# Performance work log

Hardware: AMD Instinct MI355X
Metric: run time of the kernel (lower is better)

The kernel has to match this reference:

```python
import jax, jax.numpy as jnp
import numpy as np

B, T, D = 2, 2048, 2048
NH, HD = 16, 128
Q_LAT, KV_LAT = 1024, 512
EPS = 1e-6
THETA = 10000.0


def setup_inputs() -> dict:
    key = jax.random.key(0)
    ks = jax.random.split(key, 8)
    x = jax.random.normal(ks[0], (B, T, D), dtype=jnp.float32)
    # causal additive mask, broadcast over batch/heads
    neg = jnp.finfo(jnp.float32).min
    causal = jnp.where(jnp.tril(jnp.ones((T, T), dtype=bool)), 0.0, neg)
    attn_mask = causal[None, None, :, :].astype(jnp.float32)
    s = lambda fan_in: 1.0 / np.sqrt(fan_in)
    q_a_w = jax.random.normal(ks[1], (Q_LAT, D), dtype=jnp.float32) * s(D)
    q_b_w = jax.random.normal(ks[2], (NH * HD, Q_LAT), dtype=jnp.float32) * s(Q_LAT)
    kv_a_w = jax.random.normal(ks[3], (KV_LAT, D), dtype=jnp.float32) * s(D)
    k_b_w = jax.random.normal(ks[4], (NH * HD, KV_LAT), dtype=jnp.float32) * s(KV_LAT)
    v_b_w = jax.random.normal(ks[5], (NH * HD, KV_LAT), dtype=jnp.float32) * s(KV_LAT)
    o_w = jax.random.normal(ks[6], (D, NH * HD), dtype=jnp.float32) * s(NH * HD)
    q_norm_w = jnp.ones((HD,), dtype=jnp.float32)
    k_norm_w = jnp.ones((HD,), dtype=jnp.float32)
    return dict(x=x, attn_mask=attn_mask, q_a_w=q_a_w, q_b_w=q_b_w, kv_a_w=kv_a_w,
                k_b_w=k_b_w, v_b_w=v_b_w, o_w=o_w, q_norm_w=q_norm_w, k_norm_w=k_norm_w)


def _rms_norm(x, w):
    var = jnp.mean(jnp.square(x), axis=-1, keepdims=True)
    return x * jax.lax.rsqrt(var + EPS) * w


def _rope_cache(t, hd, dtype):
    inv_freq = 1.0 / (THETA ** (jnp.arange(0, hd, 2, dtype=jnp.float32) / hd))
    freqs = jnp.arange(t, dtype=jnp.float32)[:, None] * inv_freq[None, :]  # [t, hd/2]
    emb = jnp.concatenate([freqs, freqs], axis=-1)  # [t, hd]
    return jnp.cos(emb).astype(dtype), jnp.sin(emb).astype(dtype)


def _rotate_half(x):
    h = x.shape[-1] // 2
    return jnp.concatenate([-x[..., h:], x[..., :h]], axis=-1)


def reference(x, attn_mask, q_a_w, q_b_w, kv_a_w, k_b_w, v_b_w, o_w, q_norm_w, k_norm_w):
    b, t, d = x.shape
    # low-rank projections (torch Linear: y = x @ W.T)
    q = (x @ q_a_w.T) @ q_b_w.T          # [b, t, nh*hd]
    kv = x @ kv_a_w.T                     # [b, t, kv_lat]
    k = kv @ k_b_w.T
    v = kv @ v_b_w.T
    q = q.reshape(b, t, NH, HD).transpose(0, 2, 1, 3)  # [b, nh, t, hd]
    k = k.reshape(b, t, NH, HD).transpose(0, 2, 1, 3)
    v = v.reshape(b, t, NH, HD).transpose(0, 2, 1, 3)
    # QK-norm over head dim
    q = _rms_norm(q, q_norm_w)
    k = _rms_norm(k, k_norm_w)
    # RoPE
    cos, sin = _rope_cache(t, HD, x.dtype)  # [t, hd]
    cos = cos[None, None, :, :]
    sin = sin[None, None, :, :]
    q = q * cos + _rotate_half(q) * sin
    k = k * cos + _rotate_half(k) * sin
    # attention
    sd = 1.0 / np.sqrt(HD)
    attn = jnp.einsum('bhqd,bhkd->bhqk', q, k) * sd + attn_mask
    attn = jax.nn.softmax(attn, axis=-1)
    out = jnp.einsum('bhqk,bhkd->bhqd', attn, v)
    out = out.transpose(0, 2, 1, 3).reshape(b, t, NH * HD)
    return out @ o_w.T
```

## Files before the change

kernel.cpp:

```cpp
#include <hip/hip_runtime.h>
#include <hip/hip_fp16.h>

typedef _Float16 f16;
typedef _Float16 f16x4 __attribute__((ext_vector_type(4)));
typedef _Float16 f16x8 __attribute__((ext_vector_type(8)));
typedef float f32x4 __attribute__((ext_vector_type(4)));

#define BT 4096
#define DMODEL 2048

__device__ __forceinline__ void gld16(const f16* g, f16* l) {
    __builtin_amdgcn_global_load_lds((const __attribute__((address_space(1))) void*)g,
                                     (__attribute__((address_space(3))) void*)l, 16, 0, 0);
}

struct Cvt7 {
    const float* s[7];
    f16* d[7];
    int off4[8];
};
__global__ __launch_bounds__(256) void k_cvt7(Cvt7 c) {
    int i = blockIdx.x * 256 + threadIdx.x;
    if (i >= c.off4[7]) return;
    int seg = 0;
#pragma unroll
    for (int k = 1; k < 7; ++k) seg += (i >= c.off4[k]);
    int j = i - c.off4[seg];
    float4 v = ((const float4*)c.s[seg])[j];
    f16x4 h;
    h[0] = (f16)v.x; h[1] = (f16)v.y; h[2] = (f16)v.z; h[3] = (f16)v.w;
    ((f16x4*)c.d[seg])[j] = h;
}

template <typename CT>
__global__ __launch_bounds__(256, 3) void k_gemm_bt(const f16* __restrict__ A,
                                                    const f16* __restrict__ Bm,
                                                    CT* __restrict__ C,
                                                    int M, int N, int K) {
    __shared__ __align__(16) char smem[16384];
    f16* Als = (f16*)smem;
    f16* Bls = (f16*)(smem + 8192);
    const int tid = threadIdx.x;
    const int w = tid >> 6, l = tid & 63;
    const int quad = l >> 4, ln = l & 15;
    const int m0 = blockIdx.y * 128, n0 = blockIdx.x * 128;
    const int wm = (w >> 1) * 64, wn = (w & 1) * 64;
    const int srow = l >> 2, scol = (l & 3) * 8;

    f32x4 acc[4][4];
#pragma unroll
    for (int i = 0; i < 4; ++i)
#pragma unroll
        for (int j = 0; j < 4; ++j)
#pragma unroll
            for (int r = 0; r < 4; ++r) acc[i][j][r] = 0.f;

    for (int k0 = 0; k0 < K; k0 += 32) {
#pragma unroll
        for (int c = 0; c < 2; ++c) {
            const int ch = w + 4 * c;
            gld16(A + (size_t)(m0 + ch * 16 + srow) * K + (k0 + scol), &Als[ch * 512]);
            gld16(Bm + (size_t)(n0 + ch * 16 + srow) * K + (k0 + scol), &Bls[ch * 512]);
        }
        __syncthreads();
        f16x8 af[4], bf[4];
#pragma unroll
        for (int i = 0; i < 4; ++i) af[i] = *(const f16x8*)&Als[(wm + 16 * i + ln) * 32 + quad * 8];
#pragma unroll
        for (int j = 0; j < 4; ++j) bf[j] = *(const f16x8*)&Bls[(wn + 16 * j + ln) * 32 + quad * 8];
#pragma unroll
        for (int i = 0; i < 4; ++i)
#pragma unroll
            for (int j = 0; j < 4; ++j)
                acc[i][j] = __builtin_amdgcn_mfma_f32_16x16x32_f16(af[i], bf[j], acc[i][j], 0, 0, 0);
        __syncthreads();
    }
    const int p_w = (w >> 1) ? 16 : 0;
#pragma unroll
    for (int i = 0; i < 4; ++i) {
        if constexpr (sizeof(CT) == 2) {
            f16* Cs = (f16*)smem;
#pragma unroll
            for (int j = 0; j < 4; ++j)
#pragma unroll
                for (int r = 0; r < 4; ++r)
                    Cs[(p_w + quad * 4 + r) * 136 + wn + 16 * j + ln] = (f16)acc[i][j][r];
            __syncthreads();
#pragma unroll
            for (int k2 = 0; k2 < 2; ++k2) {
                int idx = k2 * 256 + tid;
                int pr = idx >> 4, c = idx & 15;
                int rg = m0 + 16 * i + (pr & 15) + ((pr & 16) ? 64 : 0);
                *(f16x8*)&C[(size_t)rg * N + n0 + c * 8] = *(const f16x8*)&Cs[pr * 136 + c * 8];
            }
        } else {
            float* Cs = (float*)smem;
#pragma unroll
            for (int j = 0; j < 4; ++j)
#pragma unroll
                for (int r = 0; r < 4; ++r)
                    Cs[(p_w + quad * 4 + r) * 128 + wn + 16 * j + ln] = acc[i][j][r];
            __syncthreads();
#pragma unroll
            for (int k2 = 0; k2 < 4; ++k2) {
                int idx = k2 * 256 + tid;
                int pr = idx >> 5, c = idx & 31;
                int rg = m0 + 16 * i + (pr & 15) + ((pr & 16) ? 64 : 0);
                *(float4*)&C[(size_t)rg * N + n0 + c * 4] = *(const float4*)&Cs[pr * 128 + c * 4];
            }
        }
        __syncthreads();
    }
}

__global__ __launch_bounds__(256, 3) void k_gemm_dual(const f16* __restrict__ A,
                                                      const f16* __restrict__ B0,
                                                      const f16* __restrict__ B1,
                                                      f16* __restrict__ C0, f16* __restrict__ C1,
                                                      int K, int nsplit, int ld0, int ld1) {
    __shared__ __align__(16) char smem[16384];
    f16* Als = (f16*)smem;
    f16* Bls = (f16*)(smem + 8192);
    const int tid = threadIdx.x;
    const int w = tid >> 6, l = tid & 63;
    const int quad = l >> 4, ln = l & 15;
    const int m0 = blockIdx.y * 128, n0 = blockIdx.x * 128;
    const int wm = (w >> 1) * 64, wn = (w & 1) * 64;
    const int srow = l >> 2, scol = (l & 3) * 8;
    const f16* Bm = (n0 < nsplit) ? B0 + (size_t)n0 * K : B1 + (size_t)(n0 - nsplit) * K;

    f32x4 acc[4][4];
#pragma unroll
    for (int i = 0; i < 4; ++i)
#pragma unroll
        for (int j = 0; j < 4; ++j)
#pragma unroll
            for (int r = 0; r < 4; ++r) acc[i][j][r] = 0.f;

    for (int k0 = 0; k0 < K; k0 += 32) {
#pragma unroll
        for (int c = 0; c < 2; ++c) {
            const int ch = w + 4 * c;
            gld16(A + (size_t)(m0 + ch * 16 + srow) * K + (k0 + scol), &Als[ch * 512]);
            gld16(Bm + (size_t)(ch * 16 + srow) * K + (k0 + scol), &Bls[ch * 512]);
        }
        __syncthreads();
        f16x8 af[4], bf[4];
#pragma unroll
        for (int i = 0; i < 4; ++i) af[i] = *(const f16x8*)&Als[(wm + 16 * i + ln) * 32 + quad * 8];
#pragma unroll
        for (int j = 0; j < 4; ++j) bf[j] = *(const f16x8*)&Bls[(wn + 16 * j + ln) * 32 + quad * 8];
#pragma unroll
        for (int i = 0; i < 4; ++i)
#pragma unroll
            for (int j = 0; j < 4; ++j)
                acc[i][j] = __builtin_amdgcn_mfma_f32_16x16x32_f16(af[i], bf[j], acc[i][j], 0, 0, 0);
        __syncthreads();
    }
    f16* Cd; int ldc, cb;
    if (n0 < nsplit) { Cd = C0; ldc = ld0; cb = n0; }
    else             { Cd = C1; ldc = ld1; cb = n0 - nsplit; }
    const int p_w = (w >> 1) ? 16 : 0;
    f16* Cs = (f16*)smem;
#pragma unroll
    for (int i = 0; i < 4; ++i) {
#pragma unroll
        for (int j = 0; j < 4; ++j)
#pragma unroll
            for (int r = 0; r < 4; ++r)
                Cs[(p_w + quad * 4 + r) * 136 + wn + 16 * j + ln] = (f16)acc[i][j][r];
        __syncthreads();
#pragma unroll
        for (int k2 = 0; k2 < 2; ++k2) {
            int idx = k2 * 256 + tid;
            int pr = idx >> 4, c = idx & 15;
            int rg = m0 + 16 * i + (pr & 15) + ((pr & 16) ? 64 : 0);
            *(f16x8*)&Cd[(size_t)rg * ldc + cb + c * 8] = *(const f16x8*)&Cs[pr * 136 + c * 8];
        }
        __syncthreads();
    }
}

__global__ __launch_bounds__(256, 3) void k_gemm_kv(const f16* __restrict__ A,
                                                    const f16* __restrict__ B0,
                                                    const f16* __restrict__ B1,
                                                    f16* __restrict__ Ck, f16* __restrict__ Vt,
                                                    int K) {
    __shared__ __align__(16) char smem[16384];
    f16* Als = (f16*)smem;
    f16* Bls = (f16*)(smem + 8192);
    const int tid = threadIdx.x;
    const int w = tid >> 6, l = tid & 63;
    const int quad = l >> 4, ln = l & 15;
    const int m0 = blockIdx.y * 128, n0 = blockIdx.x * 128;
    const int wm = (w >> 1) * 64, wn = (w & 1) * 64;
    const int srow = l >> 2, scol = (l & 3) * 8;
    const f16* Bm = (n0 < 2048) ? B0 + (size_t)n0 * K : B1 + (size_t)(n0 - 2048) * K;

    f32x4 acc[4][4];
#pragma unroll
    for (int i = 0; i < 4; ++i)
#pragma unroll
        for (int j = 0; j < 4; ++j)
#pragma unroll
            for (int r = 0; r < 4; ++r) acc[i][j][r] = 0.f;

    for (int k0 = 0; k0 < K; k0 += 32) {
#pragma unroll
        for (int c = 0; c < 2; ++c) {
            const int ch = w + 4 * c;
            gld16(A + (size_t)(m0 + ch * 16 + srow) * K + (k0 + scol), &Als[ch * 512]);
            gld16(Bm + (size_t)(ch * 16 + srow) * K + (k0 + scol), &Bls[ch * 512]);
        }
        __syncthreads();
        f16x8 af[4], bf[4];
#pragma unroll
        for (int i = 0; i < 4; ++i) af[i] = *(const f16x8*)&Als[(wm + 16 * i + ln) * 32 + quad * 8];
#pragma unroll
        for (int j = 0; j < 4; ++j) bf[j] = *(const f16x8*)&Bls[(wn + 16 * j + ln) * 32 + quad * 8];
#pragma unroll
        for (int i = 0; i < 4; ++i)
#pragma unroll
            for (int j = 0; j < 4; ++j)
                acc[i][j] = __builtin_amdgcn_mfma_f32_16x16x32_f16(af[i], bf[j], acc[i][j], 0, 0, 0);
        __syncthreads();
    }
    const int p_w = (w >> 1) ? 16 : 0;
    f16* Cs = (f16*)smem;
    const int bb = m0 >> 11;
    const int tb = m0 & 2047;
#pragma unroll
    for (int i = 0; i < 4; ++i) {
#pragma unroll
        for (int j = 0; j < 4; ++j)
#pragma unroll
            for (int r = 0; r < 4; ++r)
                Cs[(p_w + quad * 4 + r) * 136 + wn + 16 * j + ln] = (f16)acc[i][j][r];
        __syncthreads();
        if (n0 < 2048) {
#pragma unroll
            for (int k2 = 0; k2 < 2; ++k2) {
                int idx = k2 * 256 + tid;
                int pr = idx >> 4, c = idx & 15;
                int rg = m0 + 16 * i + (pr & 15) + ((pr & 16) ? 64 : 0);
                *(f16x8*)&Ck[(size_t)rg * 2048 + n0 + c * 8] = *(const f16x8*)&Cs[pr * 136 + c * 8];
            }
        } else {
#pragma unroll
            for (int it = 0; it < 2; ++it) {
                int idx = it * 256 + tid;
                int d = idx & 127, tc = (idx >> 7) & 1, g = idx >> 8;
                f16x8 v;
#pragma unroll
                for (int k = 0; k < 8; ++k) v[k] = Cs[(g * 16 + tc * 8 + k) * 136 + d];
                int t = tb + 16 * i + g * 64 + tc * 8;
                *(f16x8*)&Vt[((size_t)(bb * 2048 + (n0 - 2048) + d)) * 2048 + t] = v;
            }
        }
        __syncthreads();
    }
}

__global__ __launch_bounds__(512, 2) void k_gemm8f(const f16* __restrict__ A,
                                                   const f16* __restrict__ B0,
                                                   float* __restrict__ C0,
                                                   int K, int ld0) {
    __shared__ __align__(16) f16 lds[49152];
    const int tid = threadIdx.x;
    const int w = tid >> 6, l = tid & 63;
    const int wm = w >> 2, wn = w & 3;
    const int quad = l >> 4, ln = l & 15;
    const int m0 = blockIdx.y * 128, n0 = blockIdx.x * 256;

    const f16* Bp = B0 + (size_t)n0 * K;

    const f16* ag  = A + (size_t)(m0 + w * 16 + (l >> 2)) * K + (l & 3) * 8;
    const f16* bg0 = Bp + (size_t)(w * 16 + (l >> 2)) * K + (l & 3) * 8;
    const f16* bg1 = bg0 + (size_t)128 * K;
    f16* al = &lds[w * 512];
    f16* bl = &lds[4096 + w * 512];

#define STAGE8(buf_, kc_, t_)                          \
    {                                                  \
        const int off_ = ((buf_) * 2 + (kc_)) * 12288; \
        const int g_ = (t_) * 64 + (kc_) * 32;         \
        gld16(ag + g_, al + off_);                     \
        gld16(bg0 + g_, bl + off_);                    \
        gld16(bg1 + g_, bl + off_ + 4096);             \
    }

    f32x4 acc[4][4];
#pragma unroll
    for (int i = 0; i < 4; ++i)
#pragma unroll
        for (int j = 0; j < 4; ++j)
#pragma unroll
            for (int r = 0; r < 4; ++r) acc[i][j][r] = 0.f;

    const int nt = K >> 6;
    STAGE8(0, 0, 0);
    STAGE8(0, 1, 0);
    STAGE8(1, 0, 1);
    asm volatile("s_waitcnt vmcnt(3)" ::: "memory");
    __builtin_amdgcn_s_barrier();
    asm volatile("s_waitcnt lgkmcnt(0)" ::: "memory");

    for (int t = 0; t < nt; ++t) {
        const int buf = t & 1;
#pragma unroll
        for (int kc = 0; kc < 2; ++kc) {
            const f16* Ah = &lds[(buf * 2 + kc) * 12288];
            const f16* Bh = Ah + 4096;
            f16x8 a[4], b[4];
#pragma unroll
            for (int i = 0; i < 4; ++i)
                a[i] = *(const f16x8*)&Ah[(wm * 64 + i * 16 + ln) * 32 + quad * 8];
#pragma unroll
            for (int j = 0; j < 4; ++j)
                b[j] = *(const f16x8*)&Bh[(wn * 64 + j * 16 + ln) * 32 + quad * 8];
            if (kc == 0) {
                if (t + 1 < nt) STAGE8(buf ^ 1, 1, t + 1);
            } else {
                if (t + 2 < nt) STAGE8(buf, 0, t + 2);
            }
            __builtin_amdgcn_s_barrier();
            asm volatile("s_waitcnt lgkmcnt(0)" ::: "memory");
            __builtin_amdgcn_s_setprio(1);
#pragma unroll
            for (int i = 0; i < 4; ++i)
#pragma unroll
                for (int j = 0; j < 4; ++j)
                    acc[i][j] = __builtin_amdgcn_mfma_f32_16x16x32_f16(a[i], b[j], acc[i][j], 0, 0, 0);
            __builtin_amdgcn_s_setprio(0);
            if (kc == 1 && t + 1 < nt) {
                if (t + 2 < nt) asm volatile("s_waitcnt vmcnt(3)" ::: "memory");
                else            asm volatile("s_waitcnt vmcnt(0)" ::: "memory");
            }
            __builtin_amdgcn_s_barrier();
        }
    }
#undef STAGE8

    const int p = (wm ? 16 : 0) + quad * 4;
    float* Cs = (float*)lds;
#pragma unroll
    for (int i = 0; i < 4; ++i) {
        __syncthreads();
#pragma unroll
        for (int j = 0; j < 4; ++j)
#pragma unroll
            for (int r = 0; r < 4; ++r)
                Cs[(p + r) * 260 + wn * 64 + j * 16 + ln] = acc[i][j][r];
        __syncthreads();
#pragma unroll
        for (int rr = 0; rr < 4; ++rr) {
            int idx = rr * 512 + tid;
            int row = idx >> 6, c4 = idx & 63;
            int rg = m0 + i * 16 + (row & 15) + ((row & 16) ? 64 : 0);
            *(float4*)&C0[(size_t)rg * ld0 + n0 + c4 * 4] = *(const float4*)&Cs[row * 260 + c4 * 4];
        }
    }
}

__global__ __launch_bounds__(256) void k_norm_rope(f16* __restrict__ q, f16* __restrict__ k,
                                                   const float* __restrict__ qw,
                                                   const float* __restrict__ kw) {
    const int gw = blockIdx.x * 4 + (threadIdx.x >> 6);
    const int l = threadIdx.x & 63;
    const int which = gw >> 16;
    const int rh = gw & 65535;
    const int row = rh >> 4, h = rh & 15;
    f16* p = which ? k : q;
    const float* wp = which ? kw : qw;
    const float scale = which ? 1.0f : 0.08838834764831843f;
    const size_t base = (size_t)row * DMODEL + h * 128;
    float xa = (float)p[base + l];
    float xb = (float)p[base + 64 + l];
    float ss = xa * xa + xb * xb;
#pragma unroll
    for (int off = 32; off > 0; off >>= 1) ss += __shfl_xor(ss, off);
    const float rms = rsqrtf(ss * (1.0f / 128.0f) + 1e-6f);
    const float na = xa * rms * wp[l];
    const float nb = xb * rms * wp[64 + l];
    const int t = row & 2047;
    const float freq = __expf((float)l * -0.1439115683121279f);
    const float ang = (float)t * freq;
    const float c = cosf(ang), s = sinf(ang);
    p[base + l]      = (f16)((na * c - nb * s) * scale);
    p[base + 64 + l] = (f16)((nb * c + na * s) * scale);
}

__global__ __launch_bounds__(256, 3) void k_flash(const f16* __restrict__ Q, const f16* __restrict__ K,
                                                  const f16* __restrict__ Vt, f16* __restrict__ O) {
    __shared__ f16 Kl[64 * 136];
    __shared__ f16 Vl[128 * 72];
    const int h = blockIdx.x, b = blockIdx.y, mt = 31 - blockIdx.z;
    const int tid = threadIdx.x, w = tid >> 6, l64 = tid & 63;
    const int quad = l64 >> 4, ln = l64 & 15;

    f16x8 qf[4];
    {
        const int tq = mt * 64 + w * 16 + ln;
        const f16* qp = Q + (size_t)(b * 2048 + tq) * DMODEL + h * 128 + quad * 8;
#pragma unroll
        for (int kc = 0; kc < 4; ++kc) qf[kc] = *(const f16x8*)(qp + kc * 32);
    }
    f32x4 oacc[8];
#pragma unroll
    for (int ot = 0; ot < 8; ++ot)
#pragma unroll
        for (int r = 0; r < 4; ++r) oacc[ot][r] = 0.f;
    float m_r = -INFINITY, l_r = 0.f;

    const f16* kbase = K + (size_t)(b * 2048) * DMODEL + h * 128;
    const f16* vbase = Vt + (size_t)(b * 2048 + h * 128) * 2048;

    f16x8 kr[4], vr[4];
#pragma unroll
    for (int c = 0; c < 4; ++c) {
        int idx = c * 256 + tid;
        kr[c] = *(const f16x8*)(kbase + (size_t)(idx >> 4) * DMODEL + (idx & 15) * 8);
        vr[c] = *(const f16x8*)(vbase + (size_t)(idx >> 3) * 2048 + (idx & 7) * 8);
    }

    for (int j = 0; j <= mt; ++j) {
        __syncthreads();
#pragma unroll
        for (int c = 0; c < 4; ++c) {
            int idx = c * 256 + tid;
            *(f16x8*)&Kl[(idx >> 4) * 136 + (idx & 15) * 8] = kr[c];
            *(f16x8*)&Vl[(idx >> 3) * 72 + (idx & 7) * 8] = vr[c];
        }
        __syncthreads();
        if (j < mt) {
#pragma unroll
            for (int c = 0; c < 4; ++c) {
                int idx = c * 256 + tid;
                kr[c] = *(const f16x8*)(kbase + (size_t)((j + 1) * 64 + (idx >> 4)) * DMODEL + (idx & 15) * 8);
                vr[c] = *(const f16x8*)(vbase + (size_t)(idx >> 3) * 2048 + (j + 1) * 64 + (idx & 7) * 8);
            }
        }
        f32x4 sacc[4];
#pragma unroll
        for (int nt = 0; nt < 4; ++nt)
#pragma unroll
            for (int r = 0; r < 4; ++r) sacc[nt][r] = 0.f;
#pragma unroll
        for (int nt = 0; nt < 4; ++nt)
#pragma unroll
            for (int kc = 0; kc < 4; ++kc) {
                f16x8 kf = *(const f16x8*)&Kl[(nt * 16 + ln) * 136 + kc * 32 + quad * 8];
                sacc[nt] = __builtin_amdgcn_mfma_f32_16x16x32_f16(kf, qf[kc], sacc[nt], 0, 0, 0);
            }
        if (j == mt) {
#pragma unroll
            for (int nt = 0; nt < 4; ++nt)
#pragma unroll
                for (int r = 0; r < 4; ++r)
                    if (nt * 16 + quad * 4 + r > w * 16 + ln) sacc[nt][r] = -INFINITY;
        }
        float mx = -INFINITY;
#pragma unroll
        for (int nt = 0; nt < 4; ++nt)
#pragma unroll
            for (int r = 0; r < 4; ++r) mx = fmaxf(mx, sacc[nt][r]);
        mx = fmaxf(mx, __shfl_xor(mx, 16));
        mx = fmaxf(mx, __shfl_xor(mx, 32));
        const bool grow = (mx > m_r + 8.f);
        const float mn = grow ? fmaxf(m_r, mx) : m_r;
        const float alpha = grow ? __expf(m_r - mn) : 1.f;
        m_r = mn;
        f16x4 pa[4];
        float s0 = 0.f;
#pragma unroll
        for (int nt = 0; nt < 4; ++nt)
#pragma unroll
            for (int r = 0; r < 4; ++r) {
                float pv = __expf(sacc[nt][r] - mn);
                s0 += pv;
                pa[nt][r] = (f16)pv;
            }
        s0 += __shfl_xor(s0, 16);
        s0 += __shfl_xor(s0, 32);
        l_r = l_r * alpha + s0;
        if (__ballot(grow)) {
            float ar[4];
#pragma unroll
            for (int r = 0; r < 4; ++r) ar[r] = __shfl(alpha, (l64 & 48) | (quad * 4 + r));
#pragma unroll
            for (int ot = 0; ot < 8; ++ot)
#pragma unroll
                for (int r = 0; r < 4; ++r) oacc[ot][r] *= ar[r];
        }
#pragma unroll
        for (int nt = 0; nt < 4; ++nt)
#pragma unroll
            for (int ot = 0; ot < 8; ++ot) {
                f16x4 vf = *(const f16x4*)&Vl[(ot * 16 + ln) * 72 + nt * 16 + quad * 4];
                oacc[ot] = __builtin_amdgcn_mfma_f32_16x16x16f16(pa[nt], vf, oacc[ot], 0, 0, 0);
            }
    }
    const float inv = 1.0f / l_r;
    float ivr[4];
#pragma unroll
    for (int r = 0; r < 4; ++r) ivr[r] = __shfl(inv, (l64 & 48) | (quad * 4 + r));
    __syncthreads();
#pragma unroll
    for (int ot = 0; ot < 8; ++ot)
#pragma unroll
        for (int r = 0; r < 4; ++r)
            Kl[(w * 16 + quad * 4 + r) * 136 + ot * 16 + ln] = (f16)(oacc[ot][r] * ivr[r]);
    __syncthreads();
#pragma unroll
    for (int c = 0; c < 4; ++c) {
        int idx = c * 256 + tid;
        int row = idx >> 4, col8 = (idx & 15) * 8;
        *(f16x8*)&O[(size_t)(b * 2048 + mt * 64 + row) * DMODEL + h * 128 + col8] =
            *(const f16x8*)&Kl[row * 136 + col8];
    }
}

extern "C" void kernel_launch(void* const* d_in, const int* in_sizes, int n_in,
                              void* d_out, int out_size, void* d_ws, size_t ws_size,
                              hipStream_t stream) {
    const float* x    = (const float*)d_in[0];
    const float* qaw  = (const float*)d_in[2];
    const float* qbw  = (const float*)d_in[3];
    const float* kvaw = (const float*)d_in[4];
    const float* kbw  = (const float*)d_in[5];
    const float* vbw  = (const float*)d_in[6];
    const float* ow   = (const float*)d_in[7];
    const float* qnw  = (const float*)d_in[8];
    const float* knw  = (const float*)d_in[9];
    float* out = (float*)d_out;

    char* p = (char*)d_ws;
    auto alloc = [&](size_t elems) { f16* r = (f16*)p; p += elems * sizeof(f16); return r; };
    f16* xb   = alloc((size_t)BT * 2048);
    f16* wo   = alloc((size_t)2048 * 2048);
    f16* wqa  = alloc((size_t)1024 * 2048);
    f16* wqb  = alloc((size_t)2048 * 1024);
    f16* wkva = alloc((size_t)512 * 2048);
    f16* wkb  = alloc((size_t)2048 * 512);
    f16* wvb  = alloc((size_t)2048 * 512);
    f16* qlat = alloc((size_t)BT * 1024);
    f16* kvb  = alloc((size_t)BT * 512);
    f16* qpre = alloc((size_t)BT * 2048);
    f16* kpre = alloc((size_t)BT * 2048);
    f16* vt   = xb;
    f16* attn = wqa;

    Cvt7 c;
    c.s[0] = x;    c.d[0] = xb;
    c.s[1] = qaw;  c.d[1] = wqa;
    c.s[2] = qbw;  c.d[2] = wqb;
    c.s[3] = kvaw; c.d[3] = wkva;
    c.s[4] = kbw;  c.d[4] = wkb;
    c.s[5] = vbw;  c.d[5] = wvb;
    c.s[6] = ow;   c.d[6] = wo;
    int sz4[7] = {BT * 2048 / 4, 1024 * 2048 / 4, 2048 * 1024 / 4, 512 * 2048 / 4,
                  2048 * 512 / 4, 2048 * 512 / 4, 2048 * 2048 / 4};
    c.off4[0] = 0;
    for (int i = 0; i < 7; ++i) c.off4[i + 1] = c.off4[i] + sz4[i];
    k_cvt7<<<(c.off4[7] + 255) / 256, 256, 0, stream>>>(c);

    dim3 blk(256);
    k_gemm_dual<<<dim3(1536 / 128, BT / 128), blk, 0, stream>>>(xb, wqa, wkva, qlat, kvb, 2048, 1024, 1024, 512);
    k_gemm_bt<f16><<<dim3(2048 / 128, BT / 128), blk, 0, stream>>>(qlat, wqb, qpre, BT, 2048, 1024);
    k_gemm_kv<<<dim3(4096 / 128, BT / 128), blk, 0, stream>>>(kvb, wkb, wvb, kpre, vt, 512);
    k_norm_rope<<<32768, 256, 0, stream>>>(qpre, kpre, qnw, knw);
    k_flash<<<dim3(16, 2, 32), 256, 0, stream>>>(qpre, kpre, vt, attn);
    k_gemm8f<<<dim3(2048 / 256, BT / 128), 512, 0, stream>>>(attn, wo, out, 2048, 2048);
}
```

Before: 394.2 us.

## Route all projection GEMMs through pipelined 128x256 kernel with templated epilogues

Replaces the simple 128x128 single-buffered GEMM kernels for the Q/KV latent, Q up-projection and K/V up-projection with the templated, software-pipelined 512-thread 128x256 kernel previously used only for the output projection. Mode-specific epilogues handle the split outputs, fp16 stores via an LDS staging tile, and a direct transposed V store from registers. This aims to raise MFMA utilisation and cut per-K-step barrier stalls in the earlier GEMMs. The cost is fewer blocks for the small-N GEMM (6x32 grid) and uncoalesced 8-byte transposed V writes.

```diff
diff --git a/kernel.cpp b/kernel.cpp
--- a/kernel.cpp
+++ b/kernel.cpp
@@ -32,239 +32,13 @@
     ((f16x4*)c.d[seg])[j] = h;
 }
 
-template <typename CT>
-__global__ __launch_bounds__(256, 3) void k_gemm_bt(const f16* __restrict__ A,
-                                                    const f16* __restrict__ Bm,
-                                                    CT* __restrict__ C,
-                                                    int M, int N, int K) {
-    __shared__ __align__(16) char smem[16384];
-    f16* Als = (f16*)smem;
-    f16* Bls = (f16*)(smem + 8192);
-    const int tid = threadIdx.x;
-    const int w = tid >> 6, l = tid & 63;
-    const int quad = l >> 4, ln = l & 15;
-    const int m0 = blockIdx.y * 128, n0 = blockIdx.x * 128;
-    const int wm = (w >> 1) * 64, wn = (w & 1) * 64;
-    const int srow = l >> 2, scol = (l & 3) * 8;
-
-    f32x4 acc[4][4];
-#pragma unroll
-    for (int i = 0; i < 4; ++i)
-#pragma unroll
-        for (int j = 0; j < 4; ++j)
-#pragma unroll
-            for (int r = 0; r < 4; ++r) acc[i][j][r] = 0.f;
-
-    for (int k0 = 0; k0 < K; k0 += 32) {
-#pragma unroll
-        for (int c = 0; c < 2; ++c) {
-            const int ch = w + 4 * c;
-            gld16(A + (size_t)(m0 + ch * 16 + srow) * K + (k0 + scol), &Als[ch * 512]);
-            gld16(Bm + (size_t)(n0 + ch * 16 + srow) * K + (k0 + scol), &Bls[ch * 512]);
-        }
-        __syncthreads();
-        f16x8 af[4], bf[4];
-#pragma unroll
-        for (int i = 0; i < 4; ++i) af[i] = *(const f16x8*)&Als[(wm + 16 * i + ln) * 32 + quad * 8];
-#pragma unroll
-        for (int j = 0; j < 4; ++j) bf[j] = *(const f16x8*)&Bls[(wn + 16 * j + ln) * 32 + quad * 8];
-#pragma unroll
-        for (int i = 0; i < 4; ++i)
-#pragma unroll
-            for (int j = 0; j < 4; ++j)
-                acc[i][j] = __builtin_amdgcn_mfma_f32_16x16x32_f16(af[i], bf[j], acc[i][j], 0, 0, 0);
-        __syncthreads();
-    }
-    const int p_w = (w >> 1) ? 16 : 0;
-#pragma unroll
-    for (int i = 0; i < 4; ++i) {
-        if constexpr (sizeof(CT) == 2) {
-            f16* Cs = (f16*)smem;
-#pragma unroll
-            for (int j = 0; j < 4; ++j)
-#pragma unroll
-                for (int r = 0; r < 4; ++r)
-                    Cs[(p_w + quad * 4 + r) * 136 + wn + 16 * j + ln] = (f16)acc[i][j][r];
-            __syncthreads();
-#pragma unroll
-            for (int k2 = 0; k2 < 2; ++k2) {
-                int idx = k2 * 256 + tid;
-                int pr = idx >> 4, c = idx & 15;
-                int rg = m0 + 16 * i + (pr & 15) + ((pr & 16) ? 64 : 0);
-                *(f16x8*)&C[(size_t)rg * N + n0 + c * 8] = *(const f16x8*)&Cs[pr * 136 + c * 8];
-            }
-        } else {
-            float* Cs = (float*)smem;
-#pragma unroll
-            for (int j = 0; j < 4; ++j)
-#pragma unroll
-                for (int r = 0; r < 4; ++r)
-                    Cs[(p_w + quad * 4 + r) * 128 + wn + 16 * j + ln] = acc[i][j][r];
-            __syncthreads();
-#pragma unroll
-            for (int k2 = 0; k2 < 4; ++k2) {
-                int idx = k2 * 256 + tid;
-                int pr = idx >> 5, c = idx & 31;
-                int rg = m0 + 16 * i + (pr & 15) + ((pr & 16) ? 64 : 0);
-                *(float4*)&C[(size_t)rg * N + n0 + c * 4] = *(const float4*)&Cs[pr * 128 + c * 4];
-            }
-        }
-        __syncthreads();
-    }
-}
-
-__global__ __launch_bounds__(256, 3) void k_gemm_dual(const f16* __restrict__ A,
-                                                      const f16* __restrict__ B0,
-                                                      const f16* __restrict__ B1,
-                                                      f16* __restrict__ C0, f16* __restrict__ C1,
-                                                      int K, int nsplit, int ld0, int ld1) {
-    __shared__ __align__(16) char smem[16384];
-    f16* Als = (f16*)smem;
-    f16* Bls = (f16*)(smem + 8192);
-    const int tid = threadIdx.x;
-    const int w = tid >> 6, l = tid & 63;
-    const int quad = l >> 4, ln = l & 15;
-    const int m0 = blockIdx.y * 128, n0 = blockIdx.x * 128;
-    const int wm = (w >> 1) * 64, wn = (w & 1) * 64;
-    const int srow = l >> 2, scol = (l & 3) * 8;
-    const f16* Bm = (n0 < nsplit) ? B0 + (size_t)n0 * K : B1 + (size_t)(n0 - nsplit) * K;
-
-    f32x4 acc[4][4];
-#pragma unroll
-    for (int i = 0; i < 4; ++i)
-#pragma unroll
-        for (int j = 0; j < 4; ++j)
-#pragma unroll
-            for (int r = 0; r < 4; ++r) acc[i][j][r] = 0.f;
-
-    for (int k0 = 0; k0 < K; k0 += 32) {
-#pragma unroll
-        for (int c = 0; c < 2; ++c) {
-            const int ch = w + 4 * c;
-            gld16(A + (size_t)(m0 + ch * 16 + srow) * K + (k0 + scol), &Als[ch * 512]);
-            gld16(Bm + (size_t)(ch * 16 + srow) * K + (k0 + scol), &Bls[ch * 512]);
-        }
-        __syncthreads();
-        f16x8 af[4], bf[4];
-#pragma unroll
-        for (int i = 0; i < 4; ++i) af[i] = *(const f16x8*)&Als[(wm + 16 * i + ln) * 32 + quad * 8];
-#pragma unroll
-        for (int j = 0; j < 4; ++j) bf[j] = *(const f16x8*)&Bls[(wn + 16 * j + ln) * 32 + quad * 8];
-#pragma unroll
-        for (int i = 0; i < 4; ++i)
-#pragma unroll
-            for (int j = 0; j < 4; ++j)
-                acc[i][j] = __builtin_amdgcn_mfma_f32_16x16x32_f16(af[i], bf[j], acc[i][j], 0, 0, 0);
-        __syncthreads();
-    }
-    f16* Cd; int ldc, cb;
-    if (n0 < nsplit) { Cd = C0; ldc = ld0; cb = n0; }
-    else             { Cd = C1; ldc = ld1; cb = n0 - nsplit; }
-    const int p_w = (w >> 1) ? 16 : 0;
-    f16* Cs = (f16*)smem;
-#pragma unroll
-    for (int i = 0; i < 4; ++i) {
-#pragma unroll
-        for (int j = 0; j < 4; ++j)
-#pragma unroll
-            for (int r = 0; r < 4; ++r)
-                Cs[(p_w + quad * 4 + r) * 136 + wn + 16 * j + ln] = (f16)acc[i][j][r];
-        __syncthreads();
-#pragma unroll
-        for (int k2 = 0; k2 < 2; ++k2) {
-            int idx = k2 * 256 + tid;
-            int pr = idx >> 4, c = idx & 15;
-            int rg = m0 + 16 * i + (pr & 15) + ((pr & 16) ? 64 : 0);
-            *(f16x8*)&Cd[(size_t)rg * ldc + cb + c * 8] = *(const f16x8*)&Cs[pr * 136 + c * 8];
-        }
-        __syncthreads();
-    }
-}
-
-__global__ __launch_bounds__(256, 3) void k_gemm_kv(const f16* __restrict__ A,
-                                                    const f16* __restrict__ B0,
-                                                    const f16* __restrict__ B1,
-                                                    f16* __restrict__ Ck, f16* __restrict__ Vt,
-                                                    int K) {
-    __shared__ __align__(16) char smem[16384];
-    f16* Als = (f16*)smem;
-    f16* Bls = (f16*)(smem + 8192);
-    const int tid = threadIdx.x;
-    const int w = tid >> 6, l = tid & 63;
-    const int quad = l >> 4, ln = l & 15;
-    const int m0 = blockIdx.y * 128, n0 = blockIdx.x * 128;
-    const int wm = (w >> 1) * 64, wn = (w & 1) * 64;
-    const int srow = l >> 2, scol = (l & 3) * 8;
-    const f16* Bm = (n0 < 2048) ? B0 + (size_t)n0 * K : B1 + (size_t)(n0 - 2048) * K;
-
-    f32x4 acc[4][4];
-#pragma unroll
-    for (int i = 0; i < 4; ++i)
-#pragma unroll
-        for (int j = 0; j < 4; ++j)
-#pragma unroll
-            for (int r = 0; r < 4; ++r) acc[i][j][r] = 0.f;
-
-    for (int k0 = 0; k0 < K; k0 += 32) {
-#pragma unroll
-        for (int c = 0; c < 2; ++c) {
-            const int ch = w + 4 * c;
-            gld16(A + (size_t)(m0 + ch * 16 + srow) * K + (k0 + scol), &Als[ch * 512]);
-            gld16(Bm + (size_t)(ch * 16 + srow) * K + (k0 + scol), &Bls[ch * 512]);
-        }
-        __syncthreads();
-        f16x8 af[4], bf[4];
-#pragma unroll
-        for (int i = 0; i < 4; ++i) af[i] = *(const f16x8*)&Als[(wm + 16 * i + ln) * 32 + quad * 8];
-#pragma unroll
-        for (int j = 0; j < 4; ++j) bf[j] = *(const f16x8*)&Bls[(wn + 16 * j + ln) * 32 + quad * 8];
-#pragma unroll
-        for (int i = 0; i < 4; ++i)
-#pragma unroll
-            for (int j = 0; j < 4; ++j)
-                acc[i][j] = __builtin_amdgcn_mfma_f32_16x16x32_f16(af[i], bf[j], acc[i][j], 0, 0, 0);
-        __syncthreads();
-    }
-    const int p_w = (w >> 1) ? 16 : 0;
-    f16* Cs = (f16*)smem;
-    const int bb = m0 >> 11;
-    const int tb = m0 & 2047;
-#pragma unroll
-    for (int i = 0; i < 4; ++i) {
-#pragma unroll
-        for (int j = 0; j < 4; ++j)
-#pragma unroll
-            for (int r = 0; r < 4; ++r)
-                Cs[(p_w + quad * 4 + r) * 136 + wn + 16 * j + ln] = (f16)acc[i][j][r];
-        __syncthreads();
-        if (n0 < 2048) {
-#pragma unroll
-            for (int k2 = 0; k2 < 2; ++k2) {
-                int idx = k2 * 256 + tid;
-                int pr = idx >> 4, c = idx & 15;
-                int rg = m0 + 16 * i + (pr & 15) + ((pr & 16) ? 64 : 0);
-                *(f16x8*)&Ck[(size_t)rg * 2048 + n0 + c * 8] = *(const f16x8*)&Cs[pr * 136 + c * 8];
-            }
-        } else {
-#pragma unroll
-            for (int it = 0; it < 2; ++it) {
-                int idx = it * 256 + tid;
-                int d = idx & 127, tc = (idx >> 7) & 1, g = idx >> 8;
-                f16x8 v;
-#pragma unroll
-                for (int k = 0; k < 8; ++k) v[k] = Cs[(g * 16 + tc * 8 + k) * 136 + d];
-                int t = tb + 16 * i + g * 64 + tc * 8;
-                *(f16x8*)&Vt[((size_t)(bb * 2048 + (n0 - 2048) + d)) * 2048 + t] = v;
-            }
-        }
-        __syncthreads();
-    }
-}
-
-__global__ __launch_bounds__(512, 2) void k_gemm8f(const f16* __restrict__ A,
-                                                   const f16* __restrict__ B0,
-                                                   float* __restrict__ C0,
-                                                   int K, int ld0) {
+template <int MODE, typename CT>
+__global__ __launch_bounds__(512, 2) void k_gemm8(const f16* __restrict__ A,
+                                                  const f16* __restrict__ B0,
+                                                  const f16* __restrict__ B1,
+                                                  CT* __restrict__ C0,
+                                                  f16* __restrict__ C1,
+                                                  int K, int nsplit, int ld0, int ld1) {
     __shared__ __align__(16) f16 lds[49152];
     const int tid = threadIdx.x;
     const int w = tid >> 6, l = tid & 63;
@@ -272,7 +46,14 @@
     const int quad = l >> 4, ln = l & 15;
     const int m0 = blockIdx.y * 128, n0 = blockIdx.x * 256;
 
-    const f16* Bp = B0 + (size_t)n0 * K;
+    const f16* Bp;
+    if constexpr (MODE == 0) {
+        Bp = B0 + (size_t)n0 * K;
+    } else if constexpr (MODE == 1) {
+        Bp = (n0 < nsplit) ? B0 + (size_t)n0 * K : B1 + (size_t)(n0 - nsplit) * K;
+    } else {
+        Bp = (n0 < 2048) ? B0 + (size_t)n0 * K : B1 + (size_t)(n0 - 2048) * K;
+    }
 
     const f16* ag  = A + (size_t)(m0 + w * 16 + (l >> 2)) * K + (l & 3) * 8;
     const f16* bg0 = Bp + (size_t)(w * 16 + (l >> 2)) * K + (l & 3) * 8;
@@ -341,23 +122,72 @@
     }
 #undef STAGE8
 
+    if constexpr (MODE == 2) {
+        if (n0 >= 2048) {
+            const int d0 = n0 - 2048;
+            const int bb = m0 >> 11, tb = m0 & 2047;
+#pragma unroll
+            for (int i = 0; i < 4; ++i)
+#pragma unroll
+                for (int j = 0; j < 4; ++j) {
+                    f16x4 v;
+#pragma unroll
+                    for (int r = 0; r < 4; ++r) v[r] = (f16)acc[i][j][r];
+                    *(f16x4*)&C1[((size_t)(bb * 2048 + d0 + wn * 64 + j * 16 + ln)) * 2048 +
+                                 tb + wm * 64 + i * 16 + quad * 4] = v;
+                }
+            return;
+        }
+    }
+
+    CT* Cd; int ldc; int cb;
+    if constexpr (MODE == 0) {
+        Cd = C0; ldc = ld0; cb = n0;
+    } else if constexpr (MODE == 1) {
+        if (n0 < nsplit) { Cd = C0; ldc = ld0; cb = n0; }
+        else             { Cd = (CT*)C1; ldc = ld1; cb = n0 - nsplit; }
+    } else {
+        Cd = C0; ldc = 2048; cb = n0;
+    }
+
     const int p = (wm ? 16 : 0) + quad * 4;
-    float* Cs = (float*)lds;
-#pragma unroll
-    for (int i = 0; i < 4; ++i) {
-        __syncthreads();
-#pragma unroll
-        for (int j = 0; j < 4; ++j)
-#pragma unroll
-            for (int r = 0; r < 4; ++r)
-                Cs[(p + r) * 260 + wn * 64 + j * 16 + ln] = acc[i][j][r];
-        __syncthreads();
-#pragma unroll
-        for (int rr = 0; rr < 4; ++rr) {
-            int idx = rr * 512 + tid;
-            int row = idx >> 6, c4 = idx & 63;
-            int rg = m0 + i * 16 + (row & 15) + ((row & 16) ? 64 : 0);
-            *(float4*)&C0[(size_t)rg * ld0 + n0 + c4 * 4] = *(const float4*)&Cs[row * 260 + c4 * 4];
+    if constexpr (sizeof(CT) == 2) {
+        f16* Cs = (f16*)lds;
+#pragma unroll
+        for (int i = 0; i < 4; ++i) {
+            __syncthreads();
+#pragma unroll
+            for (int j = 0; j < 4; ++j)
+#pragma unroll
+                for (int r = 0; r < 4; ++r)
+                    Cs[(p + r) * 264 + wn * 64 + j * 16 + ln] = (f16)acc[i][j][r];
+            __syncthreads();
+#pragma unroll
+            for (int rr = 0; rr < 2; ++rr) {
+                int idx = rr * 512 + tid;
+                int row = idx >> 5, c8 = idx & 31;
+                int rg = m0 + i * 16 + (row & 15) + ((row & 16) ? 64 : 0);
+                *(f16x8*)&Cd[(size_t)rg * ldc + cb + c8 * 8] = *(const f16x8*)&Cs[row * 264 + c8 * 8];
+            }
+        }
+    } else {
+        float* Cs = (float*)lds;
+#pragma unroll
+        for (int i = 0; i < 4; ++i) {
+            __syncthreads();
+#pragma unroll
+            for (int j = 0; j < 4; ++j)
+#pragma unroll
+                for (int r = 0; r < 4; ++r)
+                    Cs[(p + r) * 260 + wn * 64 + j * 16 + ln] = acc[i][j][r];
+            __syncthreads();
+#pragma unroll
+            for (int rr = 0; rr < 4; ++rr) {
+                int idx = rr * 512 + tid;
+                int row = idx >> 6, c4 = idx & 63;
+                int rg = m0 + i * 16 + (row & 15) + ((row & 16) ? 64 : 0);
+                *(float4*)&Cd[(size_t)rg * ldc + cb + c4 * 4] = *(const float4*)&Cs[row * 260 + c4 * 4];
+            }
         }
     }
 }
@@ -564,11 +394,14 @@
     for (int i = 0; i < 7; ++i) c.off4[i + 1] = c.off4[i] + sz4[i];
     k_cvt7<<<(c.off4[7] + 255) / 256, 256, 0, stream>>>(c);
 
-    dim3 blk(256);
-    k_gemm_dual<<<dim3(1536 / 128, BT / 128), blk, 0, stream>>>(xb, wqa, wkva, qlat, kvb, 2048, 1024, 1024, 512);
-    k_gemm_bt<f16><<<dim3(2048 / 128, BT / 128), blk, 0, stream>>>(qlat, wqb, qpre, BT, 2048, 1024);
-    k_gemm_kv<<<dim3(4096 / 128, BT / 128), blk, 0, stream>>>(kvb, wkb, wvb, kpre, vt, 512);
+    k_gemm8<1, f16><<<dim3(1536 / 256, BT / 128), 512, 0, stream>>>(
+        xb, wqa, wkva, qlat, kvb, 2048, 1024, 1024, 512);
+    k_gemm8<0, f16><<<dim3(2048 / 256, BT / 128), 512, 0, stream>>>(
+        qlat, wqb, nullptr, qpre, nullptr, 1024, 0, 2048, 0);
+    k_gemm8<2, f16><<<dim3(4096 / 256, BT / 128), 512, 0, stream>>>(
+        kvb, wkb, wvb, kpre, vt, 512, 0, 0, 0);
     k_norm_rope<<<32768, 256, 0, stream>>>(qpre, kpre, qnw, knw);
     k_flash<<<dim3(16, 2, 32), 256, 0, stream>>>(qpre, kpre, vt, attn);
-    k_gemm8f<<<dim3(2048 / 256, BT / 128), 512, 0, stream>>>(attn, wo, out, 2048, 2048);
-}
+    k_gemm8<0, float><<<dim3(2048 / 256, BT / 128), 512, 0, stream>>>(
+        attn, wo, nullptr, out, nullptr, 2048, 0, 2048, 0);
+}
```

New measurement: 390.6 us. No clear change (-0.9%).
